# Kernel optimization log

Hardware: AMD Instinct MI355X
Metric: run time of the kernel (lower is better)

The kernel has to match this reference:

```python
import jax, jax.numpy as jnp
import numpy as np

B, N, T, W, H, ED, S, C, E = 16, 256, 64, 12, 64, 64, 5, 4, 2048
ALPHA = 1.0
FG = W + H  # gcn_in_channels = window_size + tgcn_hidden_dim


def setup_inputs() -> dict:
    key = jax.random.key(0)
    ks = jax.random.split(key, 26)
    rn = lambda k, shape: jax.random.normal(k, shape, jnp.float32) * 0.1
    x = jax.random.normal(ks[0], (B, N, T), jnp.float32)
    src = jax.random.randint(ks[1], (E,), 0, N)
    off = jax.random.randint(ks[2], (E,), 1, N)
    dst = (src + off) % N  # no self loops
    return {
        'x': x,
        'static_edge_weight': jax.random.uniform(ks[3], (E,), jnp.float32),
        'gsl_gconv_w': rn(ks[4], (FG, ED)), 'gsl_gconv_b': rn(ks[5], (ED,)),
        'gsl_w1': rn(ks[6], (ED, ED)), 'gsl_b1': rn(ks[7], (ED,)),
        'gsl_w2': rn(ks[8], (ED, ED)), 'gsl_b2': rn(ks[9], (ED,)),
        'wz_c': rn(ks[10], (1, H)), 'bz_c': rn(ks[11], (H,)),
        'wz_l': rn(ks[12], (2 * H, H)), 'bz_l': rn(ks[13], (H,)),
        'wr_c': rn(ks[14], (1, H)), 'br_c': rn(ks[15], (H,)),
        'wr_l': rn(ks[16], (2 * H, H)), 'br_l': rn(ks[17], (H,)),
        'wh_c': rn(ks[18], (1, H)), 'bh_c': rn(ks[19], (H,)),
        'wh_l': rn(ks[20], (2 * H, H)), 'bh_l': rn(ks[21], (H,)),
        'cls_w': rn(ks[22], (N * H, C)), 'cls_b': rn(ks[23], (C,)),
        'static_edge_index': jnp.stack([src, dst]).astype(jnp.int32),
    }


def _normalize(A):
    # GCN sym-norm with added self loops; A has zero diagonal by construction.
    Ahat = A + jnp.eye(N, dtype=A.dtype)
    deg = Ahat.sum(axis=-2)  # in-degree (PyG gcn_norm scatters weight on col)
    dinv = jnp.where(deg > 0, 1.0 / jnp.sqrt(deg), 0.0)
    return dinv[..., :, None] * Ahat * dinv[..., None, :]


def reference(x, static_edge_weight, gsl_gconv_w, gsl_gconv_b, gsl_w1, gsl_b1,
              gsl_w2, gsl_b2, wz_c, bz_c, wz_l, bz_l, wr_c, br_c, wr_l, br_l,
              wh_c, bh_c, wh_l, bh_l, cls_w, cls_b, static_edge_index):
    A_stat = jnp.zeros((N, N), jnp.float32).at[static_edge_index[0], static_edge_index[1]].add(static_edge_weight)
    An_stat = _normalize(A_stat)  # [N,N]

    # Sliding windows, left-padded with zeros to window_size W.
    xp = jnp.pad(x, ((0, 0), (0, 0), (W - 1, 0)))
    widx = jnp.arange(T)[:, None] + jnp.arange(W)[None, :]
    wins = jnp.transpose(xp[:, :, widx], (2, 0, 1, 3))      # [T,B,N,W]
    xts = jnp.transpose(x, (2, 0, 1))[..., None]            # [T,B,N,1]
    cnts = jnp.minimum(jnp.arange(T) + 1, S).astype(jnp.float32)
    idxs = jnp.arange(T) % S

    def gcn_s(X, Wm, b):  # static graph, out[j] = sum_i Anorm[i,j] (XW)[i]
        return jnp.einsum('ij,bif->bjf', An_stat, X @ Wm) + b

    def gcn_d(An, X, Wm, b):  # per-batch dynamic graph
        return jnp.einsum('bij,bif->bjf', An, X @ Wm) + b

    def step(carry, xs):
        h, Eh = carry
        win, xt, cnt, idx = xs
        It = jnp.concatenate([win, h], axis=-1)             # [B,N,W+H]
        df = gcn_s(It, gsl_gconv_w, gsl_gconv_b)
        de1 = jnp.tanh(ALPHA * (df @ gsl_w1 + gsl_b1))
        de2 = jnp.tanh(ALPHA * (df @ gsl_w2 + gsl_b2))
        M12 = jnp.einsum('bie,bje->bij', de1, de2)          # de1 @ de2^T
        Et = jax.nn.relu(jnp.tanh(ALPHA * (M12 - jnp.swapaxes(M12, -1, -2))))
        Eh = Eh.at[:, idx].set(Et)                          # ring buffer write
        Mt = Eh.sum(axis=1) / cnt                           # mean over filled slots
        An = _normalize(Mt)
        cz = gcn_d(An, xt, wz_c, bz_c)
        z = jax.nn.sigmoid(jnp.concatenate([cz, h], -1) @ wz_l + bz_l)
        cr = gcn_d(An, xt, wr_c, br_c)
        r = jax.nn.sigmoid(jnp.concatenate([cr, h], -1) @ wr_l + br_l)
        ch = gcn_d(An, xt, wh_c, bh_c)
        ht = jnp.tanh(jnp.concatenate([ch, h * r], -1) @ wh_l + bh_l)
        h = z * h + (1.0 - z) * ht
        return (h, Eh), None

    h0 = jnp.zeros((B, N, H), jnp.float32)
    Eh0 = jnp.zeros((B, S, N, N), jnp.float32)
    (hT, _), _ = jax.lax.scan(step, (h0, Eh0), (wins, xts, cnts, idxs))
    return hT.reshape(B, N * H) @ cls_w + cls_b
```

## Files before the change

### kernel.cpp

```cpp
#include <hip/hip_runtime.h>
#include <hip/hip_bf16.h>


typedef unsigned short u16;
typedef unsigned int u32;
typedef unsigned long long u64;
typedef __attribute__((ext_vector_type(8))) short bf16x8;
typedef __attribute__((ext_vector_type(4))) float f32x4;

#define B_ 16
#define N_ 256
#define T_ 64
#define W_ 12
#define S_ 5
#define E_ 2048
#define G_ 16

__device__ __forceinline__ float b2f(u16 u) {
  union { u32 i; float f; } v; v.i = ((u32)u) << 16; return v.f;
}
__device__ __forceinline__ u16 f2b(float f) {
  union { float f; u32 i; } v; v.f = f;
  u32 x = v.i; x += 0x7fff + ((x >> 16) & 1); return (u16)(x >> 16);
}
__device__ __forceinline__ float ftanh(float x) {
  float e = __expf(-2.f * fabsf(x));
  float t = (1.f - e) / (1.f + e);
  return x < 0.f ? -t : t;
}
__device__ __forceinline__ float fsigm(float x) { return 1.f / (1.f + __expf(-x)); }
__device__ __forceinline__ float cvload(const void* p, size_t i, int f) {
  return f ? ((const float*)p)[i] : b2f(((const u16*)p)[i]);
}
__device__ __forceinline__ u16 cvloadb(const void* p, size_t i, int f) {
  return f ? f2b(((const float*)p)[i]) : ((const u16*)p)[i];
}
__device__ __forceinline__ float gld(const float* p) {
  return __hip_atomic_load(p, __ATOMIC_RELAXED, __HIP_MEMORY_SCOPE_SYSTEM);
}
__device__ __forceinline__ void gst(float* p, float v) {
  __hip_atomic_store(p, v, __ATOMIC_RELAXED, __HIP_MEMORY_SCOPE_SYSTEM);
}
__device__ __forceinline__ u64 gld64(const u64* p) {
  return __hip_atomic_load(p, __ATOMIC_RELAXED, __HIP_MEMORY_SCOPE_SYSTEM);
}
__device__ __forceinline__ void gst64(u64* p, u64 v) {
  __hip_atomic_store(p, v, __ATOMIC_RELAXED, __HIP_MEMORY_SCOPE_SYSTEM);
}
__device__ __forceinline__ u32 gldu(const u32* p) {
  return __hip_atomic_load(p, __ATOMIC_RELAXED, __HIP_MEMORY_SCOPE_SYSTEM);
}
__device__ __forceinline__ f32x4 mfma16(bf16x8 a, bf16x8 b, f32x4 c) {
  return __builtin_amdgcn_mfma_f32_16x16x32_bf16(a, b, c, 0, 0, 0);
}
__device__ __forceinline__ bf16x8 ldfrag(const u16* p) { return *(const bf16x8*)p; }

struct Params {
  const void *x0, *ew0, *gw0, *gb0, *w10, *b10, *w20, *b20;
  const void *wzc0, *bzc0, *wzl0, *bzl0, *wrc0, *brc0, *wrl0, *brl0;
  const void *whc0, *bhc0, *whl0, *bhl0, *clsw0, *clsb0;
  const int* eidx;
  float *degsum, *Eh, *clspart;
  u64 *de1g, *de2g, *xTp, *hgpT;
  u32 *tags;
  void* out;
};

__device__ __forceinline__ void wtag(const u32* tg, u32 target) {
  const int k = threadIdx.x & 15;
  while (!__all((int)(gldu(&tg[k]) >= target)))
    __builtin_amdgcn_s_sleep(1);
}
__device__ __forceinline__ void wtag8(const u32* tg, int base, u32 target) {
  const int k = base + (threadIdx.x & 7);
  while (!__all((int)(gldu(&tg[k]) >= target)))
    __builtin_amdgcn_s_sleep(1);
}
__device__ __forceinline__ void ptag(u32* tg, int wg, u32 val) {
  if (threadIdx.x == 0)
    __hip_atomic_store(&tg[wg], val, __ATOMIC_RELAXED, __HIP_MEMORY_SCOPE_SYSTEM);
}

__global__ void __launch_bounds__(256, 1) dtgcn_main(Params p) {
  __shared__ __align__(16) u16 s_union[21120];
  __shared__ __align__(16) u16 s_gwF[64 * 104];
  __shared__ __align__(16) u16 s_w1T[64 * 72], s_w2T[64 * 72];
  __shared__ __align__(16) u16 s_gzT[64 * 72], s_grT[64 * 72], s_ghT[64 * 72];
  __shared__ __align__(16) u16 s_antO1[16 * 264], s_antO2[16 * 264];
  __shared__ __align__(16) u16 s_m1[16 * 104];
  __shared__ float s_msum[16 * 257];
  __shared__ __align__(16) u16 s_de1I[16 * 72], s_de2I[16 * 72];
  __shared__ __align__(16) u16 s_hbf[16 * 72];
  __shared__ __align__(16) u16 s_dfhr[16 * 72];
  __shared__ float s_colv[16], s_degacc[16];
  __shared__ float s_y[256], s_dinv[256], s_s[16];
  __shared__ float s_uv[384], s_gb[64], s_b1[64], s_b2[64];
  __shared__ int s_flag;

  const int b = blockIdx.x & 15;
  const int wg = blockIdx.x >> 4;
  const int tid = threadIdx.x;
  const int lane = tid & 63;
  const int wv = tid >> 6;
  const int l = lane & 15;
  const int quad = lane >> 4;
  const int r0 = wg * 16;

  u64* de1g = p.de1g + (size_t)b * N_ * 16;
  u64* de2g = p.de2g + (size_t)b * N_ * 16;
  u64* hgpb = p.hgpT + (size_t)b * 64 * 64;
  u64* xTw  = p.xTp + (size_t)b * 64 * 64;
  const u64* xTb = xTw;
  float* degb = p.degsum + (size_t)b * N_;
  u32* tgDe = p.tags + b * 128;
  u32* tgDg = p.tags + b * 128 + 16;
  u32* tgH  = p.tags + b * 128 + 32;
  u32* tgX  = p.tags + b * 128 + 48;
  u32* tgC  = p.tags + b * 128 + 64;

  if (tid == 0) {
    const u16* q = (const u16*)p.x0;
    int c = 0;
    for (int i = 0; i < 256; ++i) {
      int ex = (q[i] >> 7) & 0xff;
      c += (ex >= 110 && ex <= 135);
    }
    s_flag = (c < 200) ? 1 : 0;
  }
  __syncthreads();
  const int fl = s_flag;

  {
    u16* xs = s_union;
    #pragma unroll
    for (int r = 0; r < 4; ++r) {
      const int tt = wg * 4 + r;
      xs[r * 256 + tid] = f2b(cvload(p.x0, ((size_t)b * N_ + tid) * T_ + tt, fl));
    }
    __syncthreads();
    const int r = tid >> 6, c = tid & 63;
    u64 v = (u64)xs[r * 256 + 4 * c]
          | ((u64)xs[r * 256 + 4 * c + 1] << 16)
          | ((u64)xs[r * 256 + 4 * c + 2] << 32)
          | ((u64)xs[r * 256 + 4 * c + 3] << 48);
    gst64(&xTw[(size_t)(wg * 4 + r) * 64 + c], v);
    __syncthreads();
    ptag(tgX, wg, 1);
  }

  {
    float* s_acol = (float*)s_union;
    float* s_dg   = (float*)s_union + 4096;
    for (int i = tid; i < 4096; i += 256) s_acol[i] = 0.f;
    s_dg[tid] = 0.f;
    __syncthreads();
    for (int e2 = tid; e2 < E_; e2 += 256) {
      const int sN = p.eidx[e2], dN = p.eidx[E_ + e2];
      const float wv2 = cvload(p.ew0, e2, fl);
      atomicAdd(&s_dg[dN], wv2);
      const int dl = dN - r0;
      if (dl >= 0 && dl < 16) atomicAdd(&s_acol[sN * 16 + dl], wv2);
    }
    __syncthreads();
    s_dg[tid] = rsqrtf(1.f + s_dg[tid]);
    __syncthreads();
    for (int idx = tid; idx < 4096; idx += 256) {
      const int jl = idx >> 8, i = idx & 255;
      float a = s_acol[i * 16 + jl] + ((i == r0 + jl) ? 1.f : 0.f);
      float v = s_dg[i] * a * s_dg[r0 + jl];
      u16 hi = f2b(v);
      s_antO1[jl * 264 + i] = hi;
      s_antO2[jl * 264 + i] = f2b(v - b2f(hi));
    }
  }

  for (int idx = tid; idx < 64 * 104; idx += 256) {
    const int ee = idx / 104, k = idx - ee * 104;
    u16 v = 0;
    if (k < 64) v = cvloadb(p.gw0, (12 + k) * 64 + ee, fl);
    else if (k < 76) v = cvloadb(p.gw0, (k - 64) * 64 + ee, fl);
    s_gwF[ee * 104 + k] = v;
  }
  for (int idx = tid; idx < 4096; idx += 256) {
    const int ee = idx >> 6, ff = idx & 63;
    s_w1T[ee * 72 + ff] = cvloadb(p.w10, ff * 64 + ee, fl);
    s_w2T[ee * 72 + ff] = cvloadb(p.w20, ff * 64 + ee, fl);
    s_gzT[ee * 72 + ff] = cvloadb(p.wzl0, 4096 + ff * 64 + ee, fl);
    s_grT[ee * 72 + ff] = cvloadb(p.wrl0, 4096 + ff * 64 + ee, fl);
    s_ghT[ee * 72 + ff] = cvloadb(p.whl0, 4096 + ff * 64 + ee, fl);
  }
  if (tid < 64) {
    const int e2 = tid;
    float uz = 0, vz = 0, ur = 0, vr = 0, uh = 0, vh = 0;
    for (int f = 0; f < 64; ++f) {
      float wz = cvload(p.wzl0, f * 64 + e2, fl);
      float wr = cvload(p.wrl0, f * 64 + e2, fl);
      float wh = cvload(p.whl0, f * 64 + e2, fl);
      uz += cvload(p.wzc0, f, fl) * wz; vz += cvload(p.bzc0, f, fl) * wz;
      ur += cvload(p.wrc0, f, fl) * wr; vr += cvload(p.brc0, f, fl) * wr;
      uh += cvload(p.whc0, f, fl) * wh; vh += cvload(p.bhc0, f, fl) * wh;
    }
    s_uv[0 * 64 + e2] = uz; s_uv[1 * 64 + e2] = vz + cvload(p.bzl0, e2, fl);
    s_uv[2 * 64 + e2] = ur; s_uv[3 * 64 + e2] = vr + cvload(p.brl0, e2, fl);
    s_uv[4 * 64 + e2] = uh; s_uv[5 * 64 + e2] = vh + cvload(p.bhl0, e2, fl);
    s_gb[tid] = cvload(p.gb0, tid, fl);
    s_b1[tid] = cvload(p.b10, tid, fl);
    s_b2[tid] = cvload(p.b20, tid, fl);
  }
  for (int idx = tid; idx < 16 * 257; idx += 256) s_msum[idx] = 0.f;
  for (int idx = tid; idx < 16 * 72; idx += 256) s_hbf[idx] = 0;
  for (int idx = tid; idx < 16 * 104; idx += 256) s_m1[idx] = 0;
  for (int idx = 20064 + tid; idx < 21120; idx += 256) s_union[idx] = 0;
  if (tid < 16) s_degacc[tid] = 0.f;
  __syncthreads();

  u16* s_itT = s_union;
  u16* s_j1  = s_union;
  u16* s_j2  = s_union + 9216;

  float hreg[4] = {0.f, 0.f, 0.f, 0.f};
  const int e = wv * 16 + l;

  for (int t = 0; t < T_; ++t) {
    float xv;
    {
      if (t == 0) wtag(tgX, 1);
      xv = cvload(p.x0, ((size_t)b * N_ + tid) * T_ + t, fl);
      u64 tw0[2], tw1[2];
      #pragma unroll
      for (int q = 0; q < 2; ++q) {
        const int idx = q * 256 + tid;
        const int row = idx >> 5, c = idx & 31;
        const bool ok = idx < 384;
        const int tx = t - (W_ - 1) + row;
        const bool live = ok && tx >= 0;
        tw0[q] = live ? gld64(&xTb[(size_t)tx * 64 + c]) : 0ull;
        tw1[q] = live ? gld64(&xTb[(size_t)tx * 64 + 32 + c]) : 0ull;
      }
      wtag8(tgH, 0, (u32)t);
      {
        u64 th[8];
        #pragma unroll
        for (int q = 0; q < 8; ++q) {
          const int idx = q * 256 + tid;
          const int row = idx >> 5, c = idx & 31;
          th[q] = gld64(&hgpb[(size_t)row * 64 + c]);
        }
        #pragma unroll
        for (int q = 0; q < 8; ++q) {
          const int idx = q * 256 + tid;
          const int row = idx >> 5, c = idx & 31;
          *(u64*)&s_itT[row * 264 + c * 4] = th[q];
        }
        #pragma unroll
        for (int q = 0; q < 2; ++q) {
          const int idx = q * 256 + tid;
          if (idx < 384) {
            const int row = idx >> 5, c = idx & 31;
            *(u64*)&s_itT[(64 + row) * 264 + c * 4] = tw0[q];
          }
        }
      }
      __syncthreads();
      wtag8(tgH, 8, (u32)t);
      u64 th1[8];
      #pragma unroll
      for (int q = 0; q < 8; ++q) {
        const int idx = q * 256 + tid;
        const int row = idx >> 5, c = idx & 31;
        th1[q] = gld64(&hgpb[(size_t)row * 64 + 32 + c]);
      }
      f32x4 accA[2];
      accA[0] = (f32x4){0.f, 0.f, 0.f, 0.f};
      accA[1] = (f32x4){0.f, 0.f, 0.f, 0.f};
      {
        int ti = 0;
        for (int nt = wv; nt < 5; nt += 4, ++ti) {
          #pragma unroll
          for (int ch = 0; ch < 4; ++ch) {
            const int io = ch * 32 + quad * 8;
            bf16x8 bfr = ldfrag(&s_itT[(nt * 16 + l) * 264 + io]);
            accA[ti] = mfma16(ldfrag(&s_antO1[l * 264 + io]), bfr, accA[ti]);
            accA[ti] = mfma16(ldfrag(&s_antO2[l * 264 + io]), bfr, accA[ti]);
          }
        }
      }
      #pragma unroll
      for (int q = 0; q < 8; ++q) {
        const int idx = q * 256 + tid;
        const int row = idx >> 5, c = idx & 31;
        *(u64*)&s_itT[row * 264 + (32 + c) * 4] = th1[q];
      }
      #pragma unroll
      for (int q = 0; q < 2; ++q) {
        const int idx = q * 256 + tid;
        if (idx < 384) {
          const int row = idx >> 5, c = idx & 31;
          *(u64*)&s_itT[(64 + row) * 264 + (32 + c) * 4] = tw1[q];
        }
      }
      __syncthreads();
      {
        int ti = 0;
        for (int nt = wv; nt < 5; nt += 4, ++ti) {
          #pragma unroll
          for (int ch = 4; ch < 8; ++ch) {
            const int io = ch * 32 + quad * 8;
            bf16x8 bfr = ldfrag(&s_itT[(nt * 16 + l) * 264 + io]);
            accA[ti] = mfma16(ldfrag(&s_antO1[l * 264 + io]), bfr, accA[ti]);
            accA[ti] = mfma16(ldfrag(&s_antO2[l * 264 + io]), bfr, accA[ti]);
          }
          #pragma unroll
          for (int r = 0; r < 4; ++r)
            s_m1[(quad * 4 + r) * 104 + nt * 16 + l] = f2b(accA[ti][r]);
        }
      }
      __syncthreads();
      {
        f32x4 dfa = {0.f, 0.f, 0.f, 0.f};
        #pragma unroll
        for (int ks = 0; ks < 3; ++ks) {
          bf16x8 afr = ldfrag(&s_m1[l * 104 + ks * 32 + quad * 8]);
          dfa = mfma16(afr, ldfrag(&s_gwF[e * 104 + ks * 32 + quad * 8]), dfa);
        }
        #pragma unroll
        for (int r = 0; r < 4; ++r)
          s_dfhr[(quad * 4 + r) * 72 + e] = f2b(dfa[r] + s_gb[e]);
      }
      __syncthreads();
      {
        f32x4 E1, E2;
        #pragma unroll
        for (int r = 0; r < 4; ++r) { E1[r] = s_b1[e]; E2[r] = s_b2[e]; }
        #pragma unroll
        for (int ks = 0; ks < 2; ++ks) {
          bf16x8 afr = ldfrag(&s_dfhr[l * 72 + ks * 32 + quad * 8]);
          E1 = mfma16(afr, ldfrag(&s_w1T[e * 72 + ks * 32 + quad * 8]), E1);
          E2 = mfma16(afr, ldfrag(&s_w2T[e * 72 + ks * 32 + quad * 8]), E2);
        }
        #pragma unroll
        for (int r = 0; r < 4; ++r) {
          s_de1I[(quad * 4 + r) * 72 + e] = f2b(ftanh(E1[r]));
          s_de2I[(quad * 4 + r) * 72 + e] = f2b(ftanh(E2[r]));
        }
      }
      __syncthreads();
      {
        const int row = tid >> 4, c = tid & 15;
        u64 v1 = *(const u64*)&s_de1I[row * 72 + c * 4];
        u64 v2 = *(const u64*)&s_de2I[row * 72 + c * 4];
        gst64(&de1g[(size_t)(r0 + row) * 16 + c], v1);
        gst64(&de2g[(size_t)(r0 + row) * 16 + c], v2);
      }
      __syncthreads();
      ptag(tgDe, wg, (u32)(t + 1));
    }

    {
      const int sidx = t % S_;
      float* Ehc = p.Eh + ((size_t)((b * S_ + sidx) * G_ + wg)) * (N_ * 16);
      if (tid < 16) s_colv[tid] = 0.f;
      bf16x8 bq1[2], bq2[2];
      #pragma unroll
      for (int ks = 0; ks < 2; ++ks) {
        bq1[ks] = ldfrag(&s_de1I[l * 72 + ks * 32 + quad * 8]);
        bq2[ks] = ldfrag(&s_de2I[l * 72 + ks * 32 + quad * 8]);
      }
      float old0[2][4], old1[2][4];
      #pragma unroll
      for (int mt2 = 0; mt2 < 2; ++mt2) {
        const int mt = wv * 2 + mt2;
        #pragma unroll
        for (int r = 0; r < 4; ++r) {
          const int i0 = mt * 16 + quad * 4 + r;
          old0[mt2][r] = Ehc[(size_t)i0 * 16 + l];
          old1[mt2][r] = Ehc[(size_t)(128 + i0) * 16 + l];
        }
      }
      wtag8(tgDe, 0, (u32)(t + 1));
      u64 t1a[8], t2a[8];
      #pragma unroll
      for (int q = 0; q < 8; ++q) {
        const int idx = q * 256 + tid;
        const int row = idx >> 4, c = idx & 15;
        t1a[q] = gld64(&de1g[(size_t)row * 16 + c]);
        t2a[q] = gld64(&de2g[(size_t)row * 16 + c]);
      }
      #pragma unroll
      for (int q = 0; q < 8; ++q) {
        const int idx = q * 256 + tid;
        const int row = idx >> 4, c = idx & 15;
        *(u64*)&s_j1[row * 72 + c * 4] = t1a[q];
        *(u64*)&s_j2[row * 72 + c * 4] = t2a[q];
      }
      __syncthreads();
      wtag8(tgDe, 8, (u32)(t + 1));
      u64 t1b[8], t2b[8];
      #pragma unroll
      for (int q = 0; q < 8; ++q) {
        const int idx = q * 256 + tid;
        const int row = idx >> 4, c = idx & 15;
        t1b[q] = gld64(&de1g[(size_t)(128 + row) * 16 + c]);
        t2b[q] = gld64(&de2g[(size_t)(128 + row) * 16 + c]);
      }
      float dcacc = 0.f;
      #pragma unroll
      for (int mt2 = 0; mt2 < 2; ++mt2) {
        const int mt = wv * 2 + mt2;
        f32x4 D1 = {0.f, 0.f, 0.f, 0.f}, D2 = {0.f, 0.f, 0.f, 0.f};
        #pragma unroll
        for (int ks = 0; ks < 2; ++ks) {
          bf16x8 a1 = ldfrag(&s_j1[(mt * 16 + l) * 72 + ks * 32 + quad * 8]);
          bf16x8 a2 = ldfrag(&s_j2[(mt * 16 + l) * 72 + ks * 32 + quad * 8]);
          D1 = mfma16(a1, bq2[ks], D1);
          D2 = mfma16(a2, bq1[ks], D2);
        }
        #pragma unroll
        for (int r = 0; r < 4; ++r) {
          const int i = mt * 16 + quad * 4 + r;
          float d = ftanh(D1[r] - D2[r]);
          float eN = fmaxf(d, 0.f);
          float dd = eN - old0[mt2][r];
          Ehc[(size_t)i * 16 + l] = eN;
          s_msum[l * 257 + i] += dd;
          dcacc += dd;
        }
      }
      __syncthreads();
      #pragma unroll
      for (int q = 0; q < 8; ++q) {
        const int idx = q * 256 + tid;
        const int row = idx >> 4, c = idx & 15;
        *(u64*)&s_j1[row * 72 + c * 4] = t1b[q];
        *(u64*)&s_j2[row * 72 + c * 4] = t2b[q];
      }
      __syncthreads();
      #pragma unroll
      for (int mt2 = 0; mt2 < 2; ++mt2) {
        const int mt = wv * 2 + mt2;
        f32x4 D1 = {0.f, 0.f, 0.f, 0.f}, D2 = {0.f, 0.f, 0.f, 0.f};
        #pragma unroll
        for (int ks = 0; ks < 2; ++ks) {
          bf16x8 a1 = ldfrag(&s_j1[(mt * 16 + l) * 72 + ks * 32 + quad * 8]);
          bf16x8 a2 = ldfrag(&s_j2[(mt * 16 + l) * 72 + ks * 32 + quad * 8]);
          D1 = mfma16(a1, bq2[ks], D1);
          D2 = mfma16(a2, bq1[ks], D2);
        }
        #pragma unroll
        for (int r = 0; r < 4; ++r) {
          const int i = 128 + mt * 16 + quad * 4 + r;
          float d = ftanh(D1[r] - D2[r]);
          float eN = fmaxf(d, 0.f);
          float dd = eN - old1[mt2][r];
          Ehc[(size_t)i * 16 + l] = eN;
          s_msum[l * 257 + i] += dd;
          dcacc += dd;
        }
      }
      dcacc += __shfl_xor(dcacc, 16);
      dcacc += __shfl_xor(dcacc, 32);
      if (lane < 16) atomicAdd(&s_colv[lane], dcacc);
      __syncthreads();
      if (tid < 16) {
        float nd = s_degacc[tid] + s_colv[tid];
        s_degacc[tid] = nd;
        gst(&degb[r0 + tid], nd);
      }
      __syncthreads();
      ptag(tgDg, wg, (u32)(t + 1));
    }

    {
      f32x4 azh = {0.f, 0.f, 0.f, 0.f}, arh = {0.f, 0.f, 0.f, 0.f};
      #pragma unroll
      for (int ks = 0; ks < 2; ++ks) {
        bf16x8 afr = ldfrag(&s_hbf[l * 72 + ks * 32 + quad * 8]);
        azh = mfma16(afr, ldfrag(&s_gzT[e * 72 + ks * 32 + quad * 8]), azh);
        arh = mfma16(afr, ldfrag(&s_grT[e * 72 + ks * 32 + quad * 8]), arh);
      }
      wtag(tgDg, (u32)(t + 1));
      const float cnt = (float)((t + 1 < S_) ? (t + 1) : S_);
      const float invc = 1.f / cnt;
      {
        float dg = 1.f + gld(&degb[tid]) * invc;
        float di = rsqrtf(dg);
        s_dinv[tid] = di;
        s_y[tid] = di * xv;
      }
      __syncthreads();
      {
        const int jl = tid >> 4, cc = tid & 15;
        float part = 0.f;
        #pragma unroll
        for (int k = 0; k < 16; ++k) {
          const int i = cc * 16 + ((k + cc) & 15);
          part += s_msum[jl * 257 + i] * s_y[i];
        }
        part += __shfl_xor(part, 1);
        part += __shfl_xor(part, 2);
        part += __shfl_xor(part, 4);
        part += __shfl_xor(part, 8);
        if (cc == 0) {
          const int j = r0 + jl;
          s_s[jl] = s_dinv[j] * (part * invc + s_y[j]);
        }
      }
      __syncthreads();
      float sv[4];
      #pragma unroll
      for (int r = 0; r < 4; ++r) sv[r] = s_s[quad * 4 + r];
      float zz[4], rr2[4];
      #pragma unroll
      for (int r = 0; r < 4; ++r) {
        zz[r]  = fsigm(azh[r] + s_uv[0 * 64 + e] * sv[r] + s_uv[1 * 64 + e]);
        rr2[r] = fsigm(arh[r] + s_uv[2 * 64 + e] * sv[r] + s_uv[3 * 64 + e]);
      }
      #pragma unroll
      for (int r = 0; r < 4; ++r)
        s_dfhr[(quad * 4 + r) * 72 + e] = f2b(hreg[r] * rr2[r]);
      __syncthreads();
      f32x4 ah;
      #pragma unroll
      for (int r = 0; r < 4; ++r) ah[r] = s_uv[4 * 64 + e] * sv[r] + s_uv[5 * 64 + e];
      #pragma unroll
      for (int ks = 0; ks < 2; ++ks) {
        bf16x8 afr = ldfrag(&s_dfhr[l * 72 + ks * 32 + quad * 8]);
        ah = mfma16(afr, ldfrag(&s_ghT[e * 72 + ks * 32 + quad * 8]), ah);
      }
      #pragma unroll
      for (int r = 0; r < 4; ++r) {
        float ht = ftanh(ah[r]);
        hreg[r] = zz[r] * hreg[r] + (1.f - zz[r]) * ht;
      }
      {
        u16 h0 = f2b(hreg[0]), h1 = f2b(hreg[1]);
        u16 h2 = f2b(hreg[2]), h3 = f2b(hreg[3]);
        u64 hv = (u64)h0 | ((u64)h1 << 16) | ((u64)h2 << 32) | ((u64)h3 << 48);
        gst64(&hgpb[(size_t)e * 64 + (r0 >> 2) + quad], hv);
        s_hbf[(quad * 4 + 0) * 72 + e] = h0;
        s_hbf[(quad * 4 + 1) * 72 + e] = h1;
        s_hbf[(quad * 4 + 2) * 72 + e] = h2;
        s_hbf[(quad * 4 + 3) * 72 + e] = h3;
      }
      __syncthreads();
      ptag(tgH, wg, (u32)(t + 1));
    }
  }

  {
    float part[4] = {0.f, 0.f, 0.f, 0.f};
    #pragma unroll
    for (int r = 0; r < 4; ++r) {
      const size_t base = ((size_t)(r0 + quad * 4 + r) * 64 + e) * 4;
      #pragma unroll
      for (int c = 0; c < 4; ++c)
        part[c] += hreg[r] * cvload(p.clsw0, base + c, fl);
    }
    #pragma unroll
    for (int c = 0; c < 4; ++c) {
      float v = part[c];
      v += __shfl_xor(v, 1);  v += __shfl_xor(v, 2);
      v += __shfl_xor(v, 4);  v += __shfl_xor(v, 8);
      v += __shfl_xor(v, 16); v += __shfl_xor(v, 32);
      if (lane == 0) s_s[wv * 4 + c] = v;
    }
    __syncthreads();
    if (tid < 4) {
      float tot = s_s[0 + tid] + s_s[4 + tid] + s_s[8 + tid] + s_s[12 + tid];
      gst(&p.clspart[(b * 16 + wg) * 4 + tid], tot);
    }
    __syncthreads();
    ptag(tgC, wg, 1);
    if (wg == 0) {
      wtag(tgC, 1);
      if (tid < 4) {
        float v = 0.f;
        for (int k = 0; k < 16; ++k) v += gld(&p.clspart[(b * 16 + k) * 4 + tid]);
        v += cvload(p.clsb0, tid, fl);
        if (fl) ((float*)p.out)[b * 4 + tid] = v;
        else    ((u16*)p.out)[b * 4 + tid] = f2b(v);
      }
    }
  }
}

extern "C" void kernel_launch(void* const* d_in, const int* in_sizes, int n_in,
                              void* d_out, int out_size, void* d_ws, size_t ws_size,
                              hipStream_t stream) {
  float* w = (float*)d_ws;
  size_t o = 0;
  auto alloc = [&](size_t n) { float* r = w + o; o += (n + 63) & ~(size_t)63; return r; };
  u64* de1g = (u64*)alloc((size_t)B_ * N_ * 32);
  u64* de2g = (u64*)alloc((size_t)B_ * N_ * 32);
  u64* xTp  = (u64*)alloc((size_t)B_ * 64 * 128);
  float* clspart = alloc(B_ * 16 * 4);
  const size_t zero_off = o;
  u64*   hgpT  = (u64*)alloc((size_t)B_ * 64 * 128);
  float* degs  = alloc((size_t)B_ * N_);
  u32*   tags  = (u32*)alloc(B_ * 128);
  float* Eh    = alloc((size_t)B_ * S_ * N_ * N_);
  if (ws_size < o * sizeof(float)) return;

  (void)hipMemsetAsync(w + zero_off, 0, (o - zero_off) * sizeof(float), stream);

  Params p;
  p.x0  = d_in[0];  p.ew0 = d_in[1];
  p.gw0 = d_in[2];  p.gb0 = d_in[3];
  p.w10 = d_in[4];  p.b10 = d_in[5];
  p.w20 = d_in[6];  p.b20 = d_in[7];
  p.wzc0 = d_in[8];  p.bzc0 = d_in[9];  p.wzl0 = d_in[10]; p.bzl0 = d_in[11];
  p.wrc0 = d_in[12]; p.brc0 = d_in[13]; p.wrl0 = d_in[14]; p.brl0 = d_in[15];
  p.whc0 = d_in[16]; p.bhc0 = d_in[17]; p.whl0 = d_in[18]; p.bhl0 = d_in[19];
  p.clsw0 = d_in[20]; p.clsb0 = d_in[21];
  p.eidx = (const int*)d_in[22];
  p.degsum = degs; p.Eh = Eh; p.clspart = clspart;
  p.de1g = de1g; p.de2g = de2g; p.xTp = xTp; p.hgpT = hgpT;
  p.tags = tags; p.out = d_out;

  void* args[] = { &p };
  hipError_t ce = hipLaunchCooperativeKernel((const void*)dtgcn_main,
                                             dim3(B_ * G_), dim3(256), args, 0, stream);
  if (ce != hipSuccess) {
    (void)hipGetLastError();
    dtgcn_main<<<dim3(B_ * G_), dim3(256), 0, stream>>>(p);
  }
}
```

Measured before the change: 854.4 us.

## Fuse degree values with step tags, skip Eh zeroing and redundant barriers

Each degree sum is now written as a 64-bit word holding the float value and the step counter, so consumers poll the data directly instead of a separate tag array. This removes one barrier and one tag publish per step. The de1/de2 tiles are packed into registers with lane shuffles and stored to global straight from the MFMA result, which drops an LDS round trip and a barrier. Reading the old ring-buffer values is skipped until the buffer has filled, so the large Eh buffer no longer needs to be zeroed by the memset each launch. The cost is wider polling loads and correctness that depends on the warm-up step count.

```diff
diff --git a/kernel.cpp b/kernel.cpp
--- a/kernel.cpp
+++ b/kernel.cpp
@@ -60,8 +60,8 @@
   const void *wzc0, *bzc0, *wzl0, *bzl0, *wrc0, *brc0, *wrl0, *brl0;
   const void *whc0, *bhc0, *whl0, *bhl0, *clsw0, *clsb0;
   const int* eidx;
-  float *degsum, *Eh, *clspart;
-  u64 *de1g, *de2g, *xTp, *hgpT;
+  float *Eh, *clspart;
+  u64 *degsum, *de1g, *de2g, *xTp, *hgpT;
   u32 *tags;
   void* out;
 };
@@ -111,9 +111,8 @@
   u64* hgpb = p.hgpT + (size_t)b * 64 * 64;
   u64* xTw  = p.xTp + (size_t)b * 64 * 64;
   const u64* xTb = xTw;
-  float* degb = p.degsum + (size_t)b * N_;
+  u64* degb = p.degsum + (size_t)b * N_;
   u32* tgDe = p.tags + b * 128;
-  u32* tgDg = p.tags + b * 128 + 16;
   u32* tgH  = p.tags + b * 128 + 32;
   u32* tgX  = p.tags + b * 128 + 48;
   u32* tgC  = p.tags + b * 128 + 64;
@@ -338,19 +337,31 @@
           E1 = mfma16(afr, ldfrag(&s_w1T[e * 72 + ks * 32 + quad * 8]), E1);
           E2 = mfma16(afr, ldfrag(&s_w2T[e * 72 + ks * 32 + quad * 8]), E2);
         }
+        u32 v1[4], v2[4];
         #pragma unroll
         for (int r = 0; r < 4; ++r) {
-          s_de1I[(quad * 4 + r) * 72 + e] = f2b(ftanh(E1[r]));
-          s_de2I[(quad * 4 + r) * 72 + e] = f2b(ftanh(E2[r]));
-        }
-      }
-      __syncthreads();
-      {
-        const int row = tid >> 4, c = tid & 15;
-        u64 v1 = *(const u64*)&s_de1I[row * 72 + c * 4];
-        u64 v2 = *(const u64*)&s_de2I[row * 72 + c * 4];
-        gst64(&de1g[(size_t)(r0 + row) * 16 + c], v1);
-        gst64(&de2g[(size_t)(r0 + row) * 16 + c], v2);
+          v1[r] = (u32)f2b(ftanh(E1[r]));
+          v2[r] = (u32)f2b(ftanh(E2[r]));
+          s_de1I[(quad * 4 + r) * 72 + e] = (u16)v1[r];
+          s_de2I[(quad * 4 + r) * 72 + e] = (u16)v2[r];
+        }
+        #pragma unroll
+        for (int r = 0; r < 4; ++r) {
+          u32 a1 = (u32)__shfl_xor((int)v1[r], 1);
+          u32 a2 = (u32)__shfl_xor((int)v2[r], 1);
+          u32 ev1 = (l & 1) ? a1 : v1[r], od1 = (l & 1) ? v1[r] : a1;
+          u32 ev2 = (l & 1) ? a2 : v2[r], od2 = (l & 1) ? v2[r] : a2;
+          u32 w1 = ev1 | (od1 << 16), w2 = ev2 | (od2 << 16);
+          u32 x1 = (u32)__shfl_xor((int)w1, 2);
+          u32 x2 = (u32)__shfl_xor((int)w2, 2);
+          u64 q1 = (l & 2) ? ((u64)x1 | ((u64)w1 << 32)) : ((u64)w1 | ((u64)x1 << 32));
+          u64 q2 = (l & 2) ? ((u64)x2 | ((u64)w2 << 32)) : ((u64)w2 | ((u64)x2 << 32));
+          if ((l & 3) == 0) {
+            const size_t ro = (size_t)(r0 + quad * 4 + r) * 16 + wv * 4 + (l >> 2);
+            gst64(&de1g[ro], q1);
+            gst64(&de2g[ro], q2);
+          }
+        }
       }
       __syncthreads();
       ptag(tgDe, wg, (u32)(t + 1));
@@ -366,18 +377,23 @@
         bq1[ks] = ldfrag(&s_de1I[l * 72 + ks * 32 + quad * 8]);
         bq2[ks] = ldfrag(&s_de2I[l * 72 + ks * 32 + quad * 8]);
       }
-      float old0[2][4], old1[2][4];
-      #pragma unroll
-      for (int mt2 = 0; mt2 < 2; ++mt2) {
-        const int mt = wv * 2 + mt2;
-        #pragma unroll
-        for (int r = 0; r < 4; ++r) {
-          const int i0 = mt * 16 + quad * 4 + r;
-          old0[mt2][r] = Ehc[(size_t)i0 * 16 + l];
-          old1[mt2][r] = Ehc[(size_t)(128 + i0) * 16 + l];
-        }
-      }
-      wtag8(tgDe, 0, (u32)(t + 1));
+      const int havold = (t >= S_);
+      float old0[2][4] = {{0.f, 0.f, 0.f, 0.f}, {0.f, 0.f, 0.f, 0.f}};
+      float old1[2][4] = {{0.f, 0.f, 0.f, 0.f}, {0.f, 0.f, 0.f, 0.f}};
+      if (havold) {
+        #pragma unroll
+        for (int mt2 = 0; mt2 < 2; ++mt2) {
+          const int mt = wv * 2 + mt2;
+          #pragma unroll
+          for (int r = 0; r < 4; ++r) {
+            const int i0 = mt * 16 + quad * 4 + r;
+            old0[mt2][r] = Ehc[(size_t)i0 * 16 + l];
+            old1[mt2][r] = Ehc[(size_t)(128 + i0) * 16 + l];
+          }
+        }
+      }
+      const u32 dtgt = (u32)(t + 1);
+      wtag8(tgDe, 0, dtgt);
       u64 t1a[8], t2a[8];
       #pragma unroll
       for (int q = 0; q < 8; ++q) {
@@ -394,7 +410,7 @@
         *(u64*)&s_j2[row * 72 + c * 4] = t2a[q];
       }
       __syncthreads();
-      wtag8(tgDe, 8, (u32)(t + 1));
+      wtag8(tgDe, 8, dtgt);
       u64 t1b[8], t2b[8];
       #pragma unroll
       for (int q = 0; q < 8; ++q) {
@@ -464,10 +480,9 @@
       if (tid < 16) {
         float nd = s_degacc[tid] + s_colv[tid];
         s_degacc[tid] = nd;
-        gst(&degb[r0 + tid], nd);
-      }
-      __syncthreads();
-      ptag(tgDg, wg, (u32)(t + 1));
+        union { float f; u32 i; } cv; cv.f = nd;
+        gst64(&degb[r0 + tid], (u64)cv.i | ((u64)dtgt << 32));
+      }
     }
 
     {
@@ -478,11 +493,18 @@
         azh = mfma16(afr, ldfrag(&s_gzT[e * 72 + ks * 32 + quad * 8]), azh);
         arh = mfma16(afr, ldfrag(&s_grT[e * 72 + ks * 32 + quad * 8]), arh);
       }
-      wtag(tgDg, (u32)(t + 1));
+      const u32 dgt = (u32)(t + 1);
+      u64 du;
+      for (;;) {
+        du = gld64(&degb[tid]);
+        if (__all((int)((u32)(du >> 32) >= dgt))) break;
+        __builtin_amdgcn_s_sleep(1);
+      }
       const float cnt = (float)((t + 1 < S_) ? (t + 1) : S_);
       const float invc = 1.f / cnt;
       {
-        float dg = 1.f + gld(&degb[tid]) * invc;
+        union { u32 i; float f; } dv; dv.i = (u32)du;
+        float dg = 1.f + dv.f * invc;
         float di = rsqrtf(dg);
         s_dinv[tid] = di;
         s_y[tid] = di * xv;
@@ -590,15 +612,15 @@
   float* w = (float*)d_ws;
   size_t o = 0;
   auto alloc = [&](size_t n) { float* r = w + o; o += (n + 63) & ~(size_t)63; return r; };
+  u64* xTp  = (u64*)alloc((size_t)B_ * 64 * 128);
+  float* clspart = alloc(B_ * 16 * 4);
   u64* de1g = (u64*)alloc((size_t)B_ * N_ * 32);
   u64* de2g = (u64*)alloc((size_t)B_ * N_ * 32);
-  u64* xTp  = (u64*)alloc((size_t)B_ * 64 * 128);
-  float* clspart = alloc(B_ * 16 * 4);
+  float* Eh = alloc((size_t)B_ * S_ * N_ * N_);
   const size_t zero_off = o;
   u64*   hgpT  = (u64*)alloc((size_t)B_ * 64 * 128);
-  float* degs  = alloc((size_t)B_ * N_);
+  u64*   degs  = (u64*)alloc((size_t)B_ * N_ * 2);
   u32*   tags  = (u32*)alloc(B_ * 128);
-  float* Eh    = alloc((size_t)B_ * S_ * N_ * N_);
   if (ws_size < o * sizeof(float)) return;
 
   (void)hipMemsetAsync(w + zero_off, 0, (o - zero_off) * sizeof(float), stream);
@@ -613,7 +635,8 @@
   p.whc0 = d_in[16]; p.bhc0 = d_in[17]; p.whl0 = d_in[18]; p.bhl0 = d_in[19];
   p.clsw0 = d_in[20]; p.clsb0 = d_in[21];
   p.eidx = (const int*)d_in[22];
-  p.degsum = degs; p.Eh = Eh; p.clspart = clspart;
+  p.Eh = Eh; p.clspart = clspart;
+  p.degsum = degs;
   p.de1g = de1g; p.de2g = de2g; p.xTp = xTp; p.hgpT = hgpT;
   p.tags = tags; p.out = d_out;
 
```

New measurement: 870.4 us. About the same (+1.9%).
